# Performance work log

Measured on AMD Instinct MI355X. Metric: run time of the kernel, lower is better.

## Reference

```python
import jax, jax.numpy as jnp
import numpy as np

B, S, E, D = 8, 2048, 512, 512  # batch, seq (mesh edges), elem_size, embd_size


def setup_inputs() -> dict:
    key = jax.random.key(0)
    ks = jax.random.split(key, 5)
    scale = 1.0 / np.sqrt(E)
    return {
        "x": jax.random.normal(ks[0], (B, S, E), dtype=jnp.float32),
        "Wq": jax.random.normal(ks[1], (E, D), dtype=jnp.float32) * scale,
        "bq": jax.random.normal(ks[2], (D,), dtype=jnp.float32) * 0.01,
        "Wk": jax.random.normal(ks[3], (E, D), dtype=jnp.float32) * scale,
        "bk": jax.random.normal(ks[4], (D,), dtype=jnp.float32) * 0.01,
    }


def reference(x, Wq, bq, Wk, bk):
    elem_size = x.shape[-1]
    q = jax.nn.relu(x @ Wq + bq)              # [B,S,D]
    k = jax.nn.relu(x @ Wk + bk)              # [B,S,D]
    scores = jnp.einsum("bqd,bkd->bqk", q, k) / (elem_size ** 0.5)  # [B,S,S]
    # nn.Softmax(dim=1): normalize over the QUERY axis (column-wise softmax)
    attn = jax.nn.softmax(scores, axis=1)
    new_values = jnp.einsum("bqk,bke->bqe", attn, x)  # V = raw x (use_V=False)
    return x + new_values                     # residual connection
```

## Files before the change

### kernel.cpp

```cpp
#include <hip/hip_runtime.h>
#include <hip/hip_bf16.h>
#include <math.h>

#define Bb 8
#define Ss 2048
#define Ee 512
#define Dd 512
#define QSPLIT 16

typedef __bf16 bf16x8 __attribute__((ext_vector_type(8)));
typedef __bf16 bf16x4 __attribute__((ext_vector_type(4)));
typedef float f32x4 __attribute__((ext_vector_type(4)));


__device__ __forceinline__ void stage64(ushort* lds, const __bf16* gbase,
                                        int ldg, int wave, int lane) {
#pragma unroll
    for (int t = 0; t < 4; ++t) {
        const int slot = wave * 256 + t * 64 + lane;
        const int row  = slot >> 3;
        const int c    = (slot & 7) ^ (row & 7);
        __builtin_amdgcn_global_load_lds(
            (const __attribute__((address_space(1))) void*)(gbase + (size_t)row * ldg + c * 8),
            (__attribute__((address_space(3))) void*)(lds + (size_t)slot * 8),
            16, 0, 0);
    }
}

__device__ __forceinline__ void stage64h(ushort* lds, const __bf16* gbase,
                                         int ldg, int wave, int lane) {
#pragma unroll
    for (int t = 0; t < 2; ++t) {
        const int slot = wave * 128 + t * 64 + lane;
        const int row  = slot >> 3;
        const int c    = (slot & 7) ^ (row & 7);
        __builtin_amdgcn_global_load_lds(
            (const __attribute__((address_space(1))) void*)(gbase + (size_t)row * ldg + c * 8),
            (__attribute__((address_space(3))) void*)(lds + (size_t)slot * 8),
            16, 0, 0);
    }
}

__device__ __forceinline__ void stage32(ushort* lds, const __bf16* gbase,
                                        int ldg, int wave, int lane) {
#pragma unroll
    for (int t = 0; t < 2; ++t) {
        const int slot = wave * 128 + t * 64 + lane;
        const int row  = slot >> 2;
        const int c    = (slot & 3) ^ ((row >> 1) & 3);
        __builtin_amdgcn_global_load_lds(
            (const __attribute__((address_space(1))) void*)(gbase + (size_t)row * ldg + c * 8),
            (__attribute__((address_space(3))) void*)(lds + (size_t)slot * 8),
            16, 0, 0);
    }
}

__global__ __launch_bounds__(256) void prep_fused(
    const float* __restrict__ x,
    const float* __restrict__ Wq, const float* __restrict__ Wk,
    __bf16* __restrict__ xb, __bf16* __restrict__ xT,
    __bf16* __restrict__ WqT, __bf16* __restrict__ WkT)
{
    __shared__ float tile[64][65];
    const int bid = blockIdx.x;
    const int tid = threadIdx.x;
    if (bid < 2048) {
        const int e0 = (bid & 7) * 64;
        const int s0 = ((bid >> 3) & 31) * 64;
        const int b  = bid >> 8;
        const float* ip = x + (size_t)b * Ss * Ee;
        __bf16* xbp = xb + (size_t)b * Ss * Ee;
        __bf16* xTp = xT + (size_t)b * Ee * Ss;
        const int rrow = tid >> 4;
        const int c4   = (tid & 15) * 4;
        #pragma unroll
        for (int it = 0; it < 4; ++it) {
            const int r = it * 16 + rrow;
            const float4 v = *(const float4*)&ip[(size_t)(s0 + r) * Ee + e0 + c4];
            bf16x4 h;
            h[0] = (__bf16)v.x; h[1] = (__bf16)v.y; h[2] = (__bf16)v.z; h[3] = (__bf16)v.w;
            *(bf16x4*)&xbp[(size_t)(s0 + r) * Ee + e0 + c4] = h;
            tile[r][c4 + 0] = v.x; tile[r][c4 + 1] = v.y;
            tile[r][c4 + 2] = v.z; tile[r][c4 + 3] = v.w;
        }
        __syncthreads();
        const int sc  = (tid & 7) * 8;
        const int erb = tid >> 3;
        #pragma unroll
        for (int it = 0; it < 2; ++it) {
            const int er = it * 32 + erb;
            bf16x8 o;
            #pragma unroll
            for (int t = 0; t < 8; ++t) o[t] = (__bf16)tile[sc + t][er];
            *(bf16x8*)&xTp[(size_t)(e0 + er) * Ss + s0 + sc] = o;
        }
    } else {
        const int t  = bid - 2048;
        const float* in = (t >> 8) ? Wk : Wq;
        __bf16* outp    = (t >> 8) ? WkT : WqT;
        const int x0 = (t & 15) * 32;
        const int y0 = ((t >> 4) & 15) * 32;
        const int tx = tid & 31, ty = tid >> 5;
        for (int i = ty; i < 32; i += 8)
            tile[i][tx] = in[(size_t)(y0 + i) * 512 + (x0 + tx)];
        __syncthreads();
        for (int i = ty; i < 32; i += 8)
            outp[(size_t)(x0 + i) * 512 + (y0 + tx)] = (__bf16)tile[tx][i];
    }
}

__global__ __launch_bounds__(256, 4) void proj_kernel(
    const __bf16* __restrict__ X,
    const __bf16* __restrict__ WqT, const __bf16* __restrict__ WkT,
    const float* __restrict__ bq, const float* __restrict__ bk,
    __bf16* __restrict__ qb, __bf16* __restrict__ kb)
{
    __shared__ __align__(16) ushort smem[4 * 128 * 32];
    ushort* As0 = smem;
    ushort* Bs0 = smem + 4096;
    ushort* As1 = smem + 8192;
    ushort* Bs1 = smem + 12288;
    const __bf16* WT  = blockIdx.z ? WkT : WqT;
    const float* bias = blockIdx.z ? bk : bq;
    __bf16* Out       = blockIdx.z ? kb : qb;

    const int tid = threadIdx.x;
    const int wave = tid >> 6, lane = tid & 63, quad = lane >> 4, l16 = lane & 15;
    const int wm = (wave >> 1) * 64, wn = (wave & 1) * 64;
    const int m0 = blockIdx.y * 128, n0 = blockIdx.x * 128;
    const int K = 512;
    const int swk = (quad ^ ((l16 >> 1) & 3)) * 8;

    f32x4 acc[4][4];
    f32x4 zero = {0.f, 0.f, 0.f, 0.f};
    for (int i = 0; i < 4; i++) for (int j = 0; j < 4; j++) acc[i][j] = zero;

    stage32(As0, X  + (size_t)m0 * K, K, wave, lane);
    stage32(Bs0, WT + (size_t)n0 * K, K, wave, lane);
    #pragma unroll 2
    for (int t = 0; t < 16; ++t) {
        ushort* Ac = (t & 1) ? As1 : As0;
        ushort* Bc = (t & 1) ? Bs1 : Bs0;
        if (t < 15) {
            ushort* An = (t & 1) ? As0 : As1;
            ushort* Bn = (t & 1) ? Bs0 : Bs1;
            const int kn = (t + 1) * 32;
            stage32(An, X  + (size_t)m0 * K + kn, K, wave, lane);
            stage32(Bn, WT + (size_t)n0 * K + kn, K, wave, lane);
            asm volatile("s_waitcnt vmcnt(4)" ::: "memory");
        } else {
            asm volatile("s_waitcnt vmcnt(0)" ::: "memory");
        }
        __builtin_amdgcn_s_barrier();
        bf16x8 af[4], bfr[4];
        for (int i = 0; i < 4; i++) af[i]  = *(bf16x8*)&Ac[(wm + i * 16 + l16) * 32 + swk];
        for (int j = 0; j < 4; j++) bfr[j] = *(bf16x8*)&Bc[(wn + j * 16 + l16) * 32 + swk];
        for (int i = 0; i < 4; i++)
            for (int j = 0; j < 4; j++)
                acc[i][j] = __builtin_amdgcn_mfma_f32_16x16x32_bf16(af[i], bfr[j], acc[i][j], 0, 0, 0);
        __builtin_amdgcn_sched_barrier(0);
        __builtin_amdgcn_s_barrier();
    }

    ushort* patch = smem + wave * 4096;
    for (int j = 0; j < 4; j++) {
        const float bv = bias[n0 + wn + j * 16 + l16];
        const int colsw = (j * 16 + l16) ^ (quad * 16);
        for (int i = 0; i < 4; i++)
            for (int rr = 0; rr < 4; rr++) {
                float v = acc[i][j][rr] + bv;
                v = v > 0.f ? v : 0.f;
                patch[(i * 16 + quad * 4 + rr) * 64 + colsw] = ((ushort2*)&v)[0].y;
            }
    }
    __syncthreads();
    #pragma unroll
    for (int it = 0; it < 8; it++) {
        const int lr = it * 8 + (lane >> 3);
        const int lc = ((lane & 7) * 8) ^ (((lr >> 2) & 3) * 16);
        const bf16x8 v = *(const bf16x8*)&patch[lr * 64 + lc];
        *(bf16x8*)&Out[(size_t)(m0 + wm + lr) * 512 + n0 + wn + (((lane & 7) * 8))] = v;
    }
}

__global__ __launch_bounds__(256, 4) void scores_kernel(
    const __bf16* __restrict__ Q,
    const __bf16* __restrict__ Km,
    __bf16* __restrict__ P,
    float* __restrict__ Lp)
{
    __shared__ __align__(16) ushort smem[2 * 128 * 64];
    __shared__ float stats[256];
    ushort* As = smem;
    ushort* Bs = smem + 128 * 64;
    const int id = blockIdx.x;
    const int b = id & 7;
    const int rest = id >> 3;
    const int qy = rest >> 4;
    const int m0 = qy * 128;
    const int n0 = (rest & 15) * 128;
    const __bf16* A  = Q  + (size_t)b * Ss * Dd;
    const __bf16* Bp = Km + (size_t)b * Ss * Dd;
    __bf16* C = P + (size_t)b * Ss * Ss;

    const int tid = threadIdx.x;
    const int wave = tid >> 6, lane = tid & 63, quad = lane >> 4, l16 = lane & 15;
    const int wm = (wave >> 1) * 64, wn = (wave & 1) * 64;
    const int sw0 = ((quad)     ^ (l16 & 7)) * 8;
    const int sw1 = ((quad + 4) ^ (l16 & 7)) * 8;
    const float scale = 0.044194173824159216f;
    const float SHIFT = 8.0f;

    f32x4 acc[4][4];
    f32x4 zero = {0.f, 0.f, 0.f, 0.f};
    for (int i = 0; i < 4; i++) for (int j = 0; j < 4; j++) acc[i][j] = zero;

    for (int k0 = 0; k0 < Dd; k0 += 64) {
        stage64(As, A  + (size_t)m0 * Dd + k0, Dd, wave, lane);
        stage64(Bs, Bp + (size_t)n0 * Dd + k0, Dd, wave, lane);
        __syncthreads();
        #pragma unroll
        for (int h = 0; h < 2; h++) {
            const int sw = h ? sw1 : sw0;
            bf16x8 af[4], bfr[4];
            for (int i = 0; i < 4; i++) af[i]  = *(bf16x8*)&As[(wm + i * 16 + l16) * 64 + sw];
            for (int j = 0; j < 4; j++) bfr[j] = *(bf16x8*)&Bs[(wn + j * 16 + l16) * 64 + sw];
            for (int i = 0; i < 4; i++)
                for (int j = 0; j < 4; j++)
                    acc[i][j] = __builtin_amdgcn_mfma_f32_16x16x32_bf16(af[i], bfr[j], acc[i][j], 0, 0, 0);
        }
        __syncthreads();
    }

    float* Ls = stats;
    const int half = wave >> 1;
    ushort* patch = smem + wave * 4096;
    float lj[4];
    for (int j = 0; j < 4; j++) {
        float l = 0.f;
        const int colsw = (j * 16 + l16) ^ (quad * 16);
        for (int i = 0; i < 4; i++)
            for (int rr = 0; rr < 4; rr++) {
                const float e = __expf(fmaf(acc[i][j][rr], scale, -SHIFT));
                const __bf16 pb = (__bf16)e;
                patch[(i * 16 + quad * 4 + rr) * 64 + colsw] = *(const ushort*)&pb;
                l += e;
            }
        l += __shfl_xor(l, 16);
        l += __shfl_xor(l, 32);
        lj[j] = l;
    }
    if (quad == 0)
        for (int j = 0; j < 4; j++) Ls[half * 128 + wn + j * 16 + l16] = lj[j];
    __syncthreads();
    if (tid < 128) {
        const size_t o = ((size_t)qy * Bb + b) * Ss + n0 + tid;
        Lp[o] = Ls[tid] + Ls[128 + tid];
    }
    #pragma unroll
    for (int it = 0; it < 8; it++) {
        const int lr = it * 8 + (lane >> 3);
        const int lc = ((lane & 7) * 8) ^ (((lr >> 2) & 3) * 16);
        const bf16x8 v = *(const bf16x8*)&patch[lr * 64 + lc];
        *(bf16x8*)&C[(size_t)(m0 + wm + lr) * Ss + n0 + wn + ((lane & 7) * 8)] = v;
    }
}

__global__ __launch_bounds__(256) void csx_kernel(const float* __restrict__ Lp,
                                                  const __bf16* __restrict__ xT,
                                                  __bf16* __restrict__ XC) {
    __shared__ float cinv[2048];
    const int b = blockIdx.x >> 6;
    const int g = blockIdx.x & 63;
    const int tid = threadIdx.x;
    const int k0 = tid * 8;
    float s[8];
    #pragma unroll
    for (int u = 0; u < 8; ++u) s[u] = 0.f;
    for (int qy = 0; qy < QSPLIT; ++qy) {
        const float* lp = Lp + ((size_t)qy * Bb + b) * Ss + k0;
        const float4 a0 = *(const float4*)lp;
        const float4 a1 = *(const float4*)(lp + 4);
        s[0] += a0.x; s[1] += a0.y; s[2] += a0.z; s[3] += a0.w;
        s[4] += a1.x; s[5] += a1.y; s[6] += a1.z; s[7] += a1.w;
    }
    #pragma unroll
    for (int u = 0; u < 8; ++u) cinv[k0 + u] = 1.0f / s[u];
    __syncthreads();
    const float4 c0 = *(const float4*)&cinv[k0];
    const float4 c1 = *(const float4*)&cinv[k0 + 4];
    #pragma unroll
    for (int r = 0; r < 8; ++r) {
        const int e = g * 8 + r;
        const size_t base = ((size_t)b * Ee + e) * Ss;
        const bf16x8 v = *(const bf16x8*)&xT[base + k0];
        bf16x8 o;
        o[0] = (__bf16)((float)v[0] * c0.x);
        o[1] = (__bf16)((float)v[1] * c0.y);
        o[2] = (__bf16)((float)v[2] * c0.z);
        o[3] = (__bf16)((float)v[3] * c0.w);
        o[4] = (__bf16)((float)v[4] * c1.x);
        o[5] = (__bf16)((float)v[5] * c1.y);
        o[6] = (__bf16)((float)v[6] * c1.z);
        o[7] = (__bf16)((float)v[7] * c1.w);
        *(bf16x8*)&XC[base + k0] = o;
    }
}

__global__ __launch_bounds__(256, 4) void pv_kernel(
    const __bf16* __restrict__ P,
    const __bf16* __restrict__ XC,
    const __bf16* __restrict__ XB,
    float* __restrict__ Out)
{
    __shared__ __align__(16) ushort smem[64 * 64 + 128 * 64];
    ushort* As = smem;
    ushort* Bs = smem + 64 * 64;
    const int id = blockIdx.x;
    const int b = id & 7;
    const int rest = id >> 3;
    const int m0 = (rest >> 2) * 64;
    const int n0 = (rest & 3) * 128;
    const __bf16* A  = P  + (size_t)b * Ss * Ss;
    const __bf16* Bp = XC + (size_t)b * Ee * Ss;

    const int tid = threadIdx.x;
    const int wave = tid >> 6, lane = tid & 63, quad = lane >> 4, l16 = lane & 15;
    const int wm = (wave >> 1) * 32, wn = (wave & 1) * 64;
    const int sw0 = ((quad)     ^ (l16 & 7)) * 8;
    const int sw1 = ((quad + 4) ^ (l16 & 7)) * 8;

    f32x4 acc[2][4];
    f32x4 zero = {0.f, 0.f, 0.f, 0.f};
    for (int i = 0; i < 2; i++) for (int j = 0; j < 4; j++) acc[i][j] = zero;

    for (int k0 = 0; k0 < Ss; k0 += 64) {
        stage64h(As, A  + (size_t)m0 * Ss + k0, Ss, wave, lane);
        stage64 (Bs, Bp + (size_t)n0 * Ss + k0, Ss, wave, lane);
        __syncthreads();
        #pragma unroll
        for (int h = 0; h < 2; h++) {
            const int sw = h ? sw1 : sw0;
            bf16x8 af[2], bfr[4];
            for (int i = 0; i < 2; i++) af[i]  = *(bf16x8*)&As[(wm + i * 16 + l16) * 64 + sw];
            for (int j = 0; j < 4; j++) bfr[j] = *(bf16x8*)&Bs[(wn + j * 16 + l16) * 64 + sw];
            for (int i = 0; i < 2; i++)
                for (int j = 0; j < 4; j++)
                    acc[i][j] = __builtin_amdgcn_mfma_f32_16x16x32_bf16(af[i], bfr[j], acc[i][j], 0, 0, 0);
        }
        __syncthreads();
    }

    for (int i = 0; i < 2; i++) {
        for (int j = 0; j < 4; j++) {
            const int col = n0 + wn + j * 16 + l16;
            for (int rr = 0; rr < 4; rr++) {
                const int row = m0 + wm + i * 16 + quad * 4 + rr;
                const size_t idx = ((size_t)b * Ss + row) * Ee + col;
                Out[idx] = (float)XB[idx] + acc[i][j][rr];
            }
        }
    }
}

extern "C" void kernel_launch(void* const* d_in, const int* in_sizes, int n_in,
                              void* d_out, int out_size, void* d_ws, size_t ws_size,
                              hipStream_t stream) {
    const float* x  = (const float*)d_in[0];
    const float* Wq = (const float*)d_in[1];
    const float* bq = (const float*)d_in[2];
    const float* Wk = (const float*)d_in[3];
    const float* bk = (const float*)d_in[4];
    float* out = (float*)d_out;

    char* ws = (char*)d_ws;
    size_t off = 0;
    auto alloc = [&](size_t bytes) -> void* {
        void* p = ws + off;
        off += (bytes + 255) & ~(size_t)255;
        return p;
    };
    __bf16* P    = (__bf16*)alloc((size_t)Bb * Ss * Ss * 2);
    __bf16* xb   = (__bf16*)alloc((size_t)Bb * Ss * Ee * 2);
    __bf16* qb   = (__bf16*)alloc((size_t)Bb * Ss * Dd * 2);
    __bf16* kb   = (__bf16*)alloc((size_t)Bb * Ss * Dd * 2);
    __bf16* xT   = (__bf16*)alloc((size_t)Bb * Ee * Ss * 2);
    __bf16* WqT  = (__bf16*)alloc((size_t)512 * 512 * 2);
    __bf16* WkT  = (__bf16*)alloc((size_t)512 * 512 * 2);
    float*  Lp   = (float*)alloc((size_t)QSPLIT * Bb * Ss * 4);
    if (off > ws_size) return;
    __bf16* XC = qb;

    prep_fused<<<dim3(2048 + 512), 256, 0, stream>>>(x, Wq, Wk, xb, xT, WqT, WkT);

    proj_kernel<<<dim3(4, 128, 2), 256, 0, stream>>>(xb, WqT, WkT, bq, bk, qb, kb);

    scores_kernel<<<dim3(2048), 256, 0, stream>>>(qb, kb, P, Lp);

    csx_kernel<<<dim3(512), 256, 0, stream>>>(Lp, xT, XC);

    pv_kernel<<<dim3(1024), 256, 0, stream>>>(P, XC, xb, out);
}
```

Before: 206.1 us.

## Fuse column-softmax normalization into PV kernel and vectorize transpose LDS reads

Removes the separate csx kernel that scaled transposed x by inverse column sums. pv_kernel now reduces the Lp partial sums per block into LDS and scales P fragments by them before MFMA, reading xT directly. This saves a launch and the intermediate XC round trip, but each block redundantly reads all Lp partials and adds VALU work in the inner loop. The prep transpose also changes its LDS tile layout so the read side uses vector loads.

```diff
diff --git a/kernel.cpp b/kernel.cpp
--- a/kernel.cpp
+++ b/kernel.cpp
@@ -80,8 +80,8 @@
             bf16x4 h;
             h[0] = (__bf16)v.x; h[1] = (__bf16)v.y; h[2] = (__bf16)v.z; h[3] = (__bf16)v.w;
             *(bf16x4*)&xbp[(size_t)(s0 + r) * Ee + e0 + c4] = h;
-            tile[r][c4 + 0] = v.x; tile[r][c4 + 1] = v.y;
-            tile[r][c4 + 2] = v.z; tile[r][c4 + 3] = v.w;
+            tile[c4 + 0][r] = v.x; tile[c4 + 1][r] = v.y;
+            tile[c4 + 2][r] = v.z; tile[c4 + 3][r] = v.w;
         }
         __syncthreads();
         const int sc  = (tid & 7) * 8;
@@ -89,9 +89,13 @@
         #pragma unroll
         for (int it = 0; it < 2; ++it) {
             const int er = it * 32 + erb;
+            const f32x4 a0 = *(const f32x4*)&tile[er][sc];
+            const f32x4 a1 = *(const f32x4*)&tile[er][sc + 4];
             bf16x8 o;
-            #pragma unroll
-            for (int t = 0; t < 8; ++t) o[t] = (__bf16)tile[sc + t][er];
+            o[0] = (__bf16)a0[0]; o[1] = (__bf16)a0[1];
+            o[2] = (__bf16)a0[2]; o[3] = (__bf16)a0[3];
+            o[4] = (__bf16)a1[0]; o[5] = (__bf16)a1[1];
+            o[6] = (__bf16)a1[2]; o[7] = (__bf16)a1[3];
             *(bf16x8*)&xTp[(size_t)(e0 + er) * Ss + s0 + sc] = o;
         }
     } else {
@@ -266,54 +270,15 @@
     }
 }
 
-__global__ __launch_bounds__(256) void csx_kernel(const float* __restrict__ Lp,
-                                                  const __bf16* __restrict__ xT,
-                                                  __bf16* __restrict__ XC) {
-    __shared__ float cinv[2048];
-    const int b = blockIdx.x >> 6;
-    const int g = blockIdx.x & 63;
-    const int tid = threadIdx.x;
-    const int k0 = tid * 8;
-    float s[8];
-    #pragma unroll
-    for (int u = 0; u < 8; ++u) s[u] = 0.f;
-    for (int qy = 0; qy < QSPLIT; ++qy) {
-        const float* lp = Lp + ((size_t)qy * Bb + b) * Ss + k0;
-        const float4 a0 = *(const float4*)lp;
-        const float4 a1 = *(const float4*)(lp + 4);
-        s[0] += a0.x; s[1] += a0.y; s[2] += a0.z; s[3] += a0.w;
-        s[4] += a1.x; s[5] += a1.y; s[6] += a1.z; s[7] += a1.w;
-    }
-    #pragma unroll
-    for (int u = 0; u < 8; ++u) cinv[k0 + u] = 1.0f / s[u];
-    __syncthreads();
-    const float4 c0 = *(const float4*)&cinv[k0];
-    const float4 c1 = *(const float4*)&cinv[k0 + 4];
-    #pragma unroll
-    for (int r = 0; r < 8; ++r) {
-        const int e = g * 8 + r;
-        const size_t base = ((size_t)b * Ee + e) * Ss;
-        const bf16x8 v = *(const bf16x8*)&xT[base + k0];
-        bf16x8 o;
-        o[0] = (__bf16)((float)v[0] * c0.x);
-        o[1] = (__bf16)((float)v[1] * c0.y);
-        o[2] = (__bf16)((float)v[2] * c0.z);
-        o[3] = (__bf16)((float)v[3] * c0.w);
-        o[4] = (__bf16)((float)v[4] * c1.x);
-        o[5] = (__bf16)((float)v[5] * c1.y);
-        o[6] = (__bf16)((float)v[6] * c1.z);
-        o[7] = (__bf16)((float)v[7] * c1.w);
-        *(bf16x8*)&XC[base + k0] = o;
-    }
-}
-
 __global__ __launch_bounds__(256, 4) void pv_kernel(
     const __bf16* __restrict__ P,
-    const __bf16* __restrict__ XC,
+    const float* __restrict__ Lp,
+    const __bf16* __restrict__ XT,
     const __bf16* __restrict__ XB,
     float* __restrict__ Out)
 {
     __shared__ __align__(16) ushort smem[64 * 64 + 128 * 64];
+    __shared__ float cinv[2048];
     ushort* As = smem;
     ushort* Bs = smem + 64 * 64;
     const int id = blockIdx.x;
@@ -322,7 +287,7 @@
     const int m0 = (rest >> 2) * 64;
     const int n0 = (rest & 3) * 128;
     const __bf16* A  = P  + (size_t)b * Ss * Ss;
-    const __bf16* Bp = XC + (size_t)b * Ee * Ss;
+    const __bf16* Bp = XT + (size_t)b * Ee * Ss;
 
     const int tid = threadIdx.x;
     const int wave = tid >> 6, lane = tid & 63, quad = lane >> 4, l16 = lane & 15;
@@ -330,6 +295,22 @@
     const int sw0 = ((quad)     ^ (l16 & 7)) * 8;
     const int sw1 = ((quad + 4) ^ (l16 & 7)) * 8;
 
+    {
+        const int kc = tid * 8;
+        float s[8];
+        #pragma unroll
+        for (int u = 0; u < 8; ++u) s[u] = 0.f;
+        for (int qy = 0; qy < QSPLIT; ++qy) {
+            const float* lp = Lp + ((size_t)qy * Bb + b) * Ss + kc;
+            const float4 a0 = *(const float4*)lp;
+            const float4 a1 = *(const float4*)(lp + 4);
+            s[0] += a0.x; s[1] += a0.y; s[2] += a0.z; s[3] += a0.w;
+            s[4] += a1.x; s[5] += a1.y; s[6] += a1.z; s[7] += a1.w;
+        }
+        #pragma unroll
+        for (int u = 0; u < 8; ++u) cinv[kc + u] = 1.0f / s[u];
+    }
+
     f32x4 acc[2][4];
     f32x4 zero = {0.f, 0.f, 0.f, 0.f};
     for (int i = 0; i < 2; i++) for (int j = 0; j < 4; j++) acc[i][j] = zero;
@@ -344,6 +325,21 @@
             bf16x8 af[2], bfr[4];
             for (int i = 0; i < 2; i++) af[i]  = *(bf16x8*)&As[(wm + i * 16 + l16) * 64 + sw];
             for (int j = 0; j < 4; j++) bfr[j] = *(bf16x8*)&Bs[(wn + j * 16 + l16) * 64 + sw];
+            {
+                const int kc = k0 + (h ? 32 : 0) + quad * 8;
+                const f32x4 c0v = *(const f32x4*)&cinv[kc];
+                const f32x4 c1v = *(const f32x4*)&cinv[kc + 4];
+                const float cs[8] = {c0v[0], c0v[1], c0v[2], c0v[3],
+                                     c1v[0], c1v[1], c1v[2], c1v[3]};
+                #pragma unroll
+                for (int i = 0; i < 2; i++) {
+                    bf16x8 a = af[i];
+                    #pragma unroll
+                    for (int t8 = 0; t8 < 8; ++t8)
+                        a[t8] = (__bf16)((float)a[t8] * cs[t8]);
+                    af[i] = a;
+                }
+            }
             for (int i = 0; i < 2; i++)
                 for (int j = 0; j < 4; j++)
                     acc[i][j] = __builtin_amdgcn_mfma_f32_16x16x32_bf16(af[i], bfr[j], acc[i][j], 0, 0, 0);
@@ -389,7 +385,6 @@
     __bf16* WkT  = (__bf16*)alloc((size_t)512 * 512 * 2);
     float*  Lp   = (float*)alloc((size_t)QSPLIT * Bb * Ss * 4);
     if (off > ws_size) return;
-    __bf16* XC = qb;
 
     prep_fused<<<dim3(2048 + 512), 256, 0, stream>>>(x, Wq, Wk, xb, xT, WqT, WkT);
 
@@ -397,7 +392,5 @@
 
     scores_kernel<<<dim3(2048), 256, 0, stream>>>(qb, kb, P, Lp);
 
-    csx_kernel<<<dim3(512), 256, 0, stream>>>(Lp, xT, XC);
-
-    pv_kernel<<<dim3(1024), 256, 0, stream>>>(P, XC, xb, out);
-}
+    pv_kernel<<<dim3(1024), 256, 0, stream>>>(P, Lp, xT, xb, out);
+}
```

New measurement: 216.6 us. 5.1% more time.
